# Optimization experiments

Measured on AMD Instinct MI355X. Metric: run time of the kernel, lower is better.

## Reference

```python
import jax, jax.numpy as jnp
import numpy as np

N_NODES = 100000
N_EDGES = 640000
IN_DIM = 64
HID = 128
NUM_GRAPHS = 128
MPNN_STEPS = 3
S2S_STEPS = 3


def setup_inputs() -> dict:
    key = jax.random.key(0)
    ks = jax.random.split(key, 20)
    x = jax.random.normal(ks[0], (N_NODES, IN_DIM), dtype=jnp.float32)
    edge_index = jax.random.randint(ks[1], (2, N_EDGES), 0, N_NODES, dtype=jnp.int32)
    batch = jnp.sort(jax.random.randint(ks[2], (N_NODES,), 0, NUM_GRAPHS, dtype=jnp.int32))
    s = 1.0 / np.sqrt(HID)
    params = {
        # input layer Linear(64 -> 128)
        'W_in': jax.random.normal(ks[3], (HID, IN_DIM), dtype=jnp.float32) * s,
        'b_in': jax.random.normal(ks[4], (HID,), dtype=jnp.float32) * s,
        # MGU parameters (torch.randn init in source)
        'W_f': jax.random.normal(ks[5], (HID, HID), dtype=jnp.float32),
        'U_f': jax.random.normal(ks[6], (HID, HID), dtype=jnp.float32),
        'b_f': jax.random.normal(ks[7], (HID,), dtype=jnp.float32),
        'W_h': jax.random.normal(ks[8], (HID, HID), dtype=jnp.float32),
        'U_h': jax.random.normal(ks[9], (HID, HID), dtype=jnp.float32),
        'b_h': jax.random.normal(ks[10], (HID,), dtype=jnp.float32),
        # Set2Set LSTM: input 2*HID, hidden HID, gate order i,f,g,o
        'lstm_w_ih': jax.random.normal(ks[11], (4 * HID, 2 * HID), dtype=jnp.float32) * s,
        'lstm_w_hh': jax.random.normal(ks[12], (4 * HID, HID), dtype=jnp.float32) * s,
        'lstm_b_ih': jax.random.normal(ks[13], (4 * HID,), dtype=jnp.float32) * s,
        'lstm_b_hh': jax.random.normal(ks[14], (4 * HID,), dtype=jnp.float32) * s,
        # prediction layer Linear(2*HID -> 1)
        'W_pred': jax.random.normal(ks[15], (1, 2 * HID), dtype=jnp.float32) * s,
        'b_pred': jax.random.normal(ks[16], (1,), dtype=jnp.float32) * s,
    }
    return {'x': x, 'edge_index': edge_index, 'batch': batch, **params}


def _mpnn_mgu(h, src, dst, W_f, U_f, b_f, W_h, U_h, b_h):
    # sum-aggregate neighbor messages: m_i = sum_{j->i} h_j
    m = jax.ops.segment_sum(h[src], dst, num_segments=N_NODES)  # [N, H]
    f_t = jax.nn.sigmoid(m @ W_f.T + h @ U_f.T + b_f)
    h_hat = jnp.tanh(m @ W_h.T + (f_t * h) @ U_h.T + b_h)
    return (1.0 - f_t) * h + f_t * h_hat


def _set2set(x, batch, w_ih, w_hh, b_ih, b_hh):
    G, H = NUM_GRAPHS, HID
    q_star = jnp.zeros((G, 2 * H), dtype=x.dtype)
    h_l = jnp.zeros((G, H), dtype=x.dtype)
    c_l = jnp.zeros((G, H), dtype=x.dtype)
    for _ in range(S2S_STEPS):
        gates = q_star @ w_ih.T + h_l @ w_hh.T + b_ih + b_hh  # [G, 4H]
        i, f, g, o = jnp.split(gates, 4, axis=-1)
        c_l = jax.nn.sigmoid(f) * c_l + jax.nn.sigmoid(i) * jnp.tanh(g)
        h_l = jax.nn.sigmoid(o) * jnp.tanh(c_l)
        q = h_l  # [G, H]
        # attention over nodes within each graph segment
        e = jnp.sum(x * q[batch], axis=-1)  # [N]
        e_max = jax.ops.segment_max(e, batch, num_segments=G)
        a_un = jnp.exp(e - e_max[batch])
        denom = jax.ops.segment_sum(a_un, batch, num_segments=G)
        a = a_un / denom[batch]
        r = jax.ops.segment_sum(a[:, None] * x, batch, num_segments=G)  # [G, H]
        q_star = jnp.concatenate([q, r], axis=-1)
    return q_star


def reference(x, edge_index, batch, W_in, b_in, W_f, U_f, b_f, W_h, U_h, b_h,
              lstm_w_ih, lstm_w_hh, lstm_b_ih, lstm_b_hh, W_pred, b_pred):
    h = jax.nn.relu(x @ W_in.T + b_in)  # [N, HID]
    src, dst = edge_index[0], edge_index[1]
    for _ in range(MPNN_STEPS):
        h = _mpnn_mgu(h, src, dst, W_f, U_f, b_f, W_h, U_h, b_h)
    q_star = _set2set(h, batch, lstm_w_ih, lstm_w_hh, lstm_b_ih, lstm_b_hh)  # [G, 2H]
    return q_star @ W_pred.T + b_pred  # [G, 1]
```

## Files before the change

kernel.cpp:

```cpp
#include <hip/hip_runtime.h>
#include <math.h>

#define N_NODES 100000
#define N_EDGES 640000
#define IN_DIM 64
#define HID 128
#define NGRAPH 128

typedef __bf16 bf16x2 __attribute__((ext_vector_type(2)));
typedef __bf16 bf16x4 __attribute__((ext_vector_type(4)));
typedef __bf16 bf16x8 __attribute__((ext_vector_type(8)));
typedef float f32x4 __attribute__((ext_vector_type(4)));

#define LDST 136

__device__ __forceinline__ float sigmoid_f(float z) {
  return __fdividef(1.f, 1.f + __expf(-z));
}
__device__ __forceinline__ float tanh_f(float z) {
  return 1.f - __fdividef(2.f, __expf(2.f * z) + 1.f);
}

__device__ __forceinline__ void fma44(const float4 A[4], const float4 B[4], float acc[4][4]) {
#pragma unroll
  for (int i2 = 0; i2 < 4; ++i2) {
    acc[i2][0] += A[i2].x*B[0].x + A[i2].y*B[1].x + A[i2].z*B[2].x + A[i2].w*B[3].x;
    acc[i2][1] += A[i2].x*B[0].y + A[i2].y*B[1].y + A[i2].z*B[2].y + A[i2].w*B[3].y;
    acc[i2][2] += A[i2].x*B[0].z + A[i2].y*B[1].z + A[i2].z*B[2].z + A[i2].w*B[3].z;
    acc[i2][3] += A[i2].x*B[0].w + A[i2].y*B[1].w + A[i2].z*B[2].w + A[i2].w*B[3].w;
  }
}

__global__ __launch_bounds__(256) void k_input(const float* __restrict__ x,
                                               const float* __restrict__ W,
                                               const float* __restrict__ b,
                                               float* __restrict__ h) {
  __shared__ float wS[64][132];
  __shared__ float xS[32][68];
  int t = threadIdx.x;
  int nb = blockIdx.x * 32;
#pragma unroll
  for (int i = 0; i < 8; ++i) {
    int idx4 = i * 256 + t;
    int j = idx4 >> 4, kq = idx4 & 15;
    float4 v = ((const float4*)W)[j * 16 + kq];
    wS[4*kq+0][j] = v.x; wS[4*kq+1][j] = v.y; wS[4*kq+2][j] = v.z; wS[4*kq+3][j] = v.w;
  }
#pragma unroll
  for (int i = 0; i < 2; ++i) {
    int idx4 = i * 256 + t;
    int n = idx4 >> 4, kq = idx4 & 15;
    float4 v = ((const float4*)x)[(nb + n) * 16 + kq];
    *((float4*)&xS[n][4*kq]) = v;
  }
  __syncthreads();
  int bq = t & 31, a = t >> 5;
  float acc[4][4] = {};
#pragma unroll
  for (int kk4 = 0; kk4 < 16; ++kk4) {
    float4 A[4], B[4];
#pragma unroll
    for (int i2 = 0; i2 < 4; ++i2) A[i2] = *((const float4*)&xS[4*a+i2][4*kk4]);
#pragma unroll
    for (int c = 0; c < 4; ++c) B[c] = *((const float4*)&wS[4*kk4+c][4*bq]);
    fma44(A, B, acc);
  }
  float4 bb = ((const float4*)b)[bq];
  float ba[4] = {bb.x, bb.y, bb.z, bb.w};
#pragma unroll
  for (int i2 = 0; i2 < 4; ++i2) {
    float4 o;
    o.x = fmaxf(acc[i2][0] + ba[0], 0.f);
    o.y = fmaxf(acc[i2][1] + ba[1], 0.f);
    o.z = fmaxf(acc[i2][2] + ba[2], 0.f);
    o.w = fmaxf(acc[i2][3] + ba[3], 0.f);
    ((float4*)h)[(nb + 4*a + i2) * 32 + bq] = o;
  }
}

__global__ __launch_bounds__(256) void k_hist(const int* __restrict__ dst,
                                              int* __restrict__ deg) {
  int e = blockIdx.x * 256 + threadIdx.x;
  if (e < N_EDGES) atomicAdd(&deg[dst[e]], 1);
}

#define SCAN_CHUNK 4096
#define SCAN_NB 25

__global__ __launch_bounds__(256) void k_scan_part(const int* __restrict__ deg,
                                                   int* __restrict__ bsum) {
  __shared__ int red[256];
  int t = threadIdx.x, b = blockIdx.x;
  int base = b * SCAN_CHUNK + t * 16;
  int s = 0;
#pragma unroll
  for (int i = 0; i < 16; ++i) {
    int idx = base + i;
    if (idx < N_NODES) s += deg[idx];
  }
  red[t] = s;
  __syncthreads();
  for (int off = 128; off > 0; off >>= 1) {
    if (t < off) red[t] += red[t + off];
    __syncthreads();
  }
  if (t == 0) bsum[b] = red[0];
}

__global__ void k_scan_mid(const int* __restrict__ bsum, int* __restrict__ boff,
                           int* __restrict__ rowstart) {
  if (threadIdx.x == 0) {
    int run = 0;
    for (int i = 0; i < SCAN_NB; ++i) { boff[i] = run; run += bsum[i]; }
    rowstart[N_NODES] = run;
  }
}

__global__ __launch_bounds__(256) void k_scan_final(const int* __restrict__ deg,
                                                    const int* __restrict__ boff,
                                                    int* __restrict__ rowstart) {
  __shared__ int ts[256];
  int t = threadIdx.x, b = blockIdx.x;
  int base = b * SCAN_CHUNK + t * 16;
  int v[16];
  int s = 0;
#pragma unroll
  for (int i = 0; i < 16; ++i) {
    int idx = base + i;
    v[i] = (idx < N_NODES) ? deg[idx] : 0;
    s += v[i];
  }
  ts[t] = s;
  __syncthreads();
  for (int off = 1; off < 256; off <<= 1) {
    int add = (t >= off) ? ts[t - off] : 0;
    __syncthreads();
    ts[t] += add;
    __syncthreads();
  }
  int run = boff[b] + ts[t] - s;
#pragma unroll
  for (int i = 0; i < 16; ++i) {
    int idx = base + i;
    if (idx < N_NODES) rowstart[idx] = run;
    run += v[i];
  }
}

__global__ __launch_bounds__(256) void k_fill(const int* __restrict__ src,
                                              const int* __restrict__ dst,
                                              int* __restrict__ cursor,
                                              int* __restrict__ srcSorted) {
  int e = blockIdx.x * 256 + threadIdx.x;
  if (e >= N_EDGES) return;
  int d = dst[e];
  int p = atomicAdd(&cursor[d], 1);
  srcSorted[p] = src[e];
}

__global__ __launch_bounds__(256) void k_wsplit(const float* __restrict__ W0,
                                                const float* __restrict__ W1,
                                                const float* __restrict__ W2,
                                                const float* __restrict__ W3,
                                                __bf16* __restrict__ Whi,
                                                __bf16* __restrict__ Wlo) {
  int id = blockIdx.x * 256 + threadIdx.x;
  int mat = id >> 14, idx = id & 16383;
  const float* W = (mat == 0) ? W0 : (mat == 1) ? W1 : (mat == 2) ? W2 : W3;
  float v = W[idx];
  __bf16 hi = (__bf16)v;
  Whi[id] = hi;
  Wlo[id] = (__bf16)(v - (float)hi);
}

__global__ __launch_bounds__(256) void k_gather(const float* __restrict__ h,
                                                const int* __restrict__ rowstart,
                                                const int* __restrict__ srcSorted,
                                                float* __restrict__ m) {
  int node = blockIdx.x * 8 + (threadIdx.x >> 5);
  if (node >= N_NODES) return;
  int li = threadIdx.x & 31;
  int j0 = rowstart[node], j1 = rowstart[node + 1];
  const float4* h4 = (const float4*)h;
  float4 a0 = {0.f, 0.f, 0.f, 0.f}, a1 = {0.f, 0.f, 0.f, 0.f};
  int j = j0;
  for (; j + 1 < j1; j += 2) {
    int s0 = srcSorted[j], s1 = srcSorted[j + 1];
    float4 v0 = h4[s0 * 32 + li];
    float4 v1 = h4[s1 * 32 + li];
    a0.x += v0.x; a0.y += v0.y; a0.z += v0.z; a0.w += v0.w;
    a1.x += v1.x; a1.y += v1.y; a1.z += v1.z; a1.w += v1.w;
  }
  if (j < j1) {
    int s0 = srcSorted[j];
    float4 v0 = h4[s0 * 32 + li];
    a0.x += v0.x; a0.y += v0.y; a0.z += v0.z; a0.w += v0.w;
  }
  float4 o = {a0.x + a1.x, a0.y + a1.y, a0.z + a1.z, a0.w + a1.w};
  ((float4*)m)[node * 32 + li] = o;
}

__global__ __launch_bounds__(256) void k_mgu(float* __restrict__ h,
                                             const float* __restrict__ m,
                                             const __bf16* __restrict__ Whi,
                                             const __bf16* __restrict__ Wlo,
                                             const float* __restrict__ bfp,
                                             const float* __restrict__ bhp) {
  __shared__ __bf16 mHi[64 * LDST], mLo[64 * LDST];
  __shared__ __bf16 hHi[64 * LDST], hLo[64 * LDST];
  const int t = threadIdx.x;
  const int nb = blockIdx.x * 64;

#pragma unroll
  for (int i = 0; i < 8; ++i) {
    int idx4 = i * 256 + t;
    int n = idx4 >> 5, kq = idx4 & 31;
    float4 vm = ((const float4*)m)[(nb + n) * 32 + kq];
    float4 vh = ((const float4*)h)[(nb + n) * 32 + kq];
    bf16x4 mh, ml, hh, hl;
    mh[0] = (__bf16)vm.x; ml[0] = (__bf16)(vm.x - (float)mh[0]);
    mh[1] = (__bf16)vm.y; ml[1] = (__bf16)(vm.y - (float)mh[1]);
    mh[2] = (__bf16)vm.z; ml[2] = (__bf16)(vm.z - (float)mh[2]);
    mh[3] = (__bf16)vm.w; ml[3] = (__bf16)(vm.w - (float)mh[3]);
    hh[0] = (__bf16)vh.x; hl[0] = (__bf16)(vh.x - (float)hh[0]);
    hh[1] = (__bf16)vh.y; hl[1] = (__bf16)(vh.y - (float)hh[1]);
    hh[2] = (__bf16)vh.z; hl[2] = (__bf16)(vh.z - (float)hh[2]);
    hh[3] = (__bf16)vh.w; hl[3] = (__bf16)(vh.w - (float)hh[3]);
    int e0 = n * LDST + 4 * kq;
    *(bf16x4*)&mHi[e0] = mh; *(bf16x4*)&mLo[e0] = ml;
    *(bf16x4*)&hHi[e0] = hh; *(bf16x4*)&hLo[e0] = hl;
  }
  __syncthreads();

  const int w = t >> 6, l = t & 63;
  const int lj = l & 15, q = l >> 4;

  float bfj[2], bhj[2];
#pragma unroll
  for (int ct = 0; ct < 2; ++ct) {
    int j = (2 * w + ct) * 16 + lj;
    bfj[ct] = bfp[j];
    bhj[ct] = bhp[j];
  }

  f32x4 acc[4][2] = {};

#pragma unroll
  for (int kc = 0; kc < 128; kc += 32) {
    bf16x8 bwh[2], bwl[2], buh[2], bul[2];
#pragma unroll
    for (int ct = 0; ct < 2; ++ct) {
      int off = ((2 * w + ct) * 16 + lj) * 128 + kc + q * 8;
      bwh[ct] = *(const bf16x8*)&Whi[off];
      bwl[ct] = *(const bf16x8*)&Wlo[off];
      buh[ct] = *(const bf16x8*)&Whi[16384 + off];
      bul[ct] = *(const bf16x8*)&Wlo[16384 + off];
    }
#pragma unroll
    for (int rt = 0; rt < 4; ++rt) {
      int e0 = (rt * 16 + lj) * LDST + kc + q * 8;
      bf16x8 amh = *(const bf16x8*)&mHi[e0];
      bf16x8 aml = *(const bf16x8*)&mLo[e0];
      bf16x8 ahh = *(const bf16x8*)&hHi[e0];
      bf16x8 ahl = *(const bf16x8*)&hLo[e0];
#pragma unroll
      for (int ct = 0; ct < 2; ++ct) {
        f32x4 a = acc[rt][ct];
        a = __builtin_amdgcn_mfma_f32_16x16x32_bf16(amh, bwh[ct], a, 0, 0, 0);
        a = __builtin_amdgcn_mfma_f32_16x16x32_bf16(amh, bwl[ct], a, 0, 0, 0);
        a = __builtin_amdgcn_mfma_f32_16x16x32_bf16(aml, bwh[ct], a, 0, 0, 0);
        a = __builtin_amdgcn_mfma_f32_16x16x32_bf16(ahh, buh[ct], a, 0, 0, 0);
        a = __builtin_amdgcn_mfma_f32_16x16x32_bf16(ahh, bul[ct], a, 0, 0, 0);
        a = __builtin_amdgcn_mfma_f32_16x16x32_bf16(ahl, buh[ct], a, 0, 0, 0);
        acc[rt][ct] = a;
      }
    }
  }

  __syncthreads();
  float fv[4][2][4], hvv[4][2][4];
#pragma unroll
  for (int rt = 0; rt < 4; ++rt)
#pragma unroll
    for (int ct = 0; ct < 2; ++ct) {
      int j = (2 * w + ct) * 16 + lj;
#pragma unroll
      for (int r = 0; r < 4; ++r) {
        int nl = rt * 16 + q * 4 + r;
        float z = acc[rt][ct][r] + bfj[ct];
        float f = sigmoid_f(z);
        int he = nl * LDST + j;
        float hval = (float)hHi[he] + (float)hLo[he];
        float g = f * hval;
        __bf16 ghi = (__bf16)g;
        hHi[he] = ghi;
        hLo[he] = (__bf16)(g - (float)ghi);
        fv[rt][ct][r] = f;
        hvv[rt][ct][r] = hval;
        acc[rt][ct][r] = 0.f;
      }
    }
  __syncthreads();

#pragma unroll
  for (int kc = 0; kc < 128; kc += 32) {
    bf16x8 bwh[2], bwl[2], buh[2], bul[2];
#pragma unroll
    for (int ct = 0; ct < 2; ++ct) {
      int off = ((2 * w + ct) * 16 + lj) * 128 + kc + q * 8;
      bwh[ct] = *(const bf16x8*)&Whi[2 * 16384 + off];
      bwl[ct] = *(const bf16x8*)&Wlo[2 * 16384 + off];
      buh[ct] = *(const bf16x8*)&Whi[3 * 16384 + off];
      bul[ct] = *(const bf16x8*)&Wlo[3 * 16384 + off];
    }
#pragma unroll
    for (int rt = 0; rt < 4; ++rt) {
      int e0 = (rt * 16 + lj) * LDST + kc + q * 8;
      bf16x8 amh = *(const bf16x8*)&mHi[e0];
      bf16x8 aml = *(const bf16x8*)&mLo[e0];
      bf16x8 agh = *(const bf16x8*)&hHi[e0];
      bf16x8 agl = *(const bf16x8*)&hLo[e0];
#pragma unroll
      for (int ct = 0; ct < 2; ++ct) {
        f32x4 a = acc[rt][ct];
        a = __builtin_amdgcn_mfma_f32_16x16x32_bf16(amh, bwh[ct], a, 0, 0, 0);
        a = __builtin_amdgcn_mfma_f32_16x16x32_bf16(amh, bwl[ct], a, 0, 0, 0);
        a = __builtin_amdgcn_mfma_f32_16x16x32_bf16(aml, bwh[ct], a, 0, 0, 0);
        a = __builtin_amdgcn_mfma_f32_16x16x32_bf16(agh, buh[ct], a, 0, 0, 0);
        a = __builtin_amdgcn_mfma_f32_16x16x32_bf16(agh, bul[ct], a, 0, 0, 0);
        a = __builtin_amdgcn_mfma_f32_16x16x32_bf16(agl, buh[ct], a, 0, 0, 0);
        acc[rt][ct] = a;
      }
    }
  }

#pragma unroll
  for (int rt = 0; rt < 4; ++rt)
#pragma unroll
    for (int ct = 0; ct < 2; ++ct) {
      int j = (2 * w + ct) * 16 + lj;
#pragma unroll
      for (int r = 0; r < 4; ++r) {
        float T = tanh_f(acc[rt][ct][r] + bhj[ct]);
        float f = fv[rt][ct][r];
        float hn = (1.f - f) * hvv[rt][ct][r] + f * T;
        h[(nb + rt * 16 + q * 4 + r) * 128 + j] = hn;
      }
    }
}

__global__ __launch_bounds__(1024) void k_s2s(const float* __restrict__ h,
                                              const int* __restrict__ batch,
                                              const float* __restrict__ w_ih,
                                              const float* __restrict__ w_hh,
                                              const float* __restrict__ b_ih,
                                              const float* __restrict__ b_hh,
                                              const float* __restrict__ Wp,
                                              const float* __restrict__ bp,
                                              float* __restrict__ out) {
  const int g = blockIdx.x, t = threadIdx.x;
  const int w = t >> 6, l = t & 63;
  const int half = l >> 5, li = l & 31;
  const int hw = 2 * w + half;
  __shared__ float qs[256];
  __shared__ float hl[128], cl[128];
  __shared__ float gates[512];
  __shared__ float redM[32], redS[32], scl[32];
  __shared__ float rPart[32][132];
  __shared__ float gInvS;
  __shared__ int bnd[2];

  if (t < 2) {
    int tgt = g + t;
    int lo = 0, hi = N_NODES;
    while (lo < hi) { int mid = (lo + hi) >> 1; if (batch[mid] < tgt) lo = mid + 1; else hi = mid; }
    bnd[t] = lo;
  }
  if (t < 256) qs[t] = 0.f;
  if (t < 128) { hl[t] = 0.f; cl[t] = 0.f; }
  __syncthreads();
  const int s0 = bnd[0], s1 = bnd[1];

  for (int step = 0; step < 3; ++step) {
#pragma unroll 2
    for (int jt = w; jt < 512; jt += 16) {
      const float* wi = w_ih + jt * 256;
      const float* wh = w_hh + jt * 128;
      float s = qs[l] * wi[l] + qs[l+64] * wi[l+64]
              + qs[l+128] * wi[l+128] + qs[l+192] * wi[l+192]
              + hl[l] * wh[l] + hl[l+64] * wh[l+64];
#pragma unroll
      for (int o = 32; o > 0; o >>= 1) s += __shfl_xor(s, o, 64);
      if (l == 0) gates[jt] = s + b_ih[jt] + b_hh[jt];
    }
    __syncthreads();
    if (t < 128) {
      float gi = gates[t], gf = gates[128 + t], gg = gates[256 + t], go = gates[384 + t];
      float c = sigmoid_f(gf) * cl[t] + sigmoid_f(gi) * tanh_f(gg);
      float hh = sigmoid_f(go) * tanh_f(c);
      cl[t] = c;
      hl[t] = hh;
      qs[t] = hh;
    }
    __syncthreads();

    float mw = -INFINITY, sw = 0.f;
    float4 racc = {0.f, 0.f, 0.f, 0.f};
    const float4* h4 = (const float4*)h;
    const float q0 = qs[4*li], q1 = qs[4*li+1], q2 = qs[4*li+2], q3 = qs[4*li+3];
    int n = s0 + hw;
    for (; n + 32 < s1; n += 64) {
      float4 hv0 = h4[n * 32 + li];
      float4 hv1 = h4[(n + 32) * 32 + li];
      float v0 = hv0.x * q0 + hv0.y * q1 + hv0.z * q2 + hv0.w * q3;
      float v1 = hv1.x * q0 + hv1.y * q1 + hv1.z * q2 + hv1.w * q3;
#pragma unroll
      for (int o = 16; o > 0; o >>= 1) {
        v0 += __shfl_xor(v0, o, 64);
        v1 += __shfl_xor(v1, o, 64);
      }
      float nm = fmaxf(mw, fmaxf(v0, v1));
      float sc = __expf(mw - nm);
      float w0 = __expf(v0 - nm);
      float w1 = __expf(v1 - nm);
      sw = sw * sc + w0 + w1;
      racc.x = racc.x * sc + w0 * hv0.x + w1 * hv1.x;
      racc.y = racc.y * sc + w0 * hv0.y + w1 * hv1.y;
      racc.z = racc.z * sc + w0 * hv0.z + w1 * hv1.z;
      racc.w = racc.w * sc + w0 * hv0.w + w1 * hv1.w;
      mw = nm;
    }
    for (; n < s1; n += 32) {
      float4 hv = h4[n * 32 + li];
      float v = hv.x * q0 + hv.y * q1 + hv.z * q2 + hv.w * q3;
#pragma unroll
      for (int o = 16; o > 0; o >>= 1) v += __shfl_xor(v, o, 64);
      float nm = fmaxf(mw, v);
      float sc = __expf(mw - nm);
      float wg = __expf(v - nm);
      sw = sw * sc + wg;
      racc.x = racc.x * sc + wg * hv.x;
      racc.y = racc.y * sc + wg * hv.y;
      racc.z = racc.z * sc + wg * hv.z;
      racc.w = racc.w * sc + wg * hv.w;
      mw = nm;
    }
    if (li == 0) { redM[hw] = mw; redS[hw] = sw; }
    *(float4*)&rPart[hw][4 * li] = racc;
    __syncthreads();
    if (t == 0) {
      float M = -INFINITY;
      for (int i = 0; i < 32; ++i) M = fmaxf(M, redM[i]);
      float S = 0.f;
      for (int i = 0; i < 32; ++i) {
        float s_ = (redM[i] > -INFINITY && M > -INFINITY) ? __expf(redM[i] - M) : 0.f;
        scl[i] = s_;
        S += redS[i] * s_;
      }
      gInvS = (S > 0.f) ? __fdividef(1.f, S) : 0.f;
    }
    __syncthreads();
    if (t < 128) {
      float inv = gInvS;
      float r = 0.f;
#pragma unroll
      for (int i = 0; i < 32; ++i) r += rPart[i][t] * scl[i];
      qs[128 + t] = r * inv;
    }
    __syncthreads();
  }

  __shared__ float pr[256];
  if (t < 256) pr[t] = qs[t] * Wp[t];
  __syncthreads();
  if (t < 128) pr[t] += pr[t + 128];
  __syncthreads();
  if (t < 64) {
    float s = pr[t] + pr[t + 64];
#pragma unroll
    for (int o = 32; o > 0; o >>= 1) s += __shfl_xor(s, o, 64);
    if (t == 0) out[g] = s + bp[0];
  }
}

extern "C" void kernel_launch(void* const* d_in, const int* in_sizes, int n_in,
                              void* d_out, int out_size, void* d_ws, size_t ws_size,
                              hipStream_t stream) {
  const float* x      = (const float*)d_in[0];
  const int*   ei     = (const int*)d_in[1];
  const int*   batch  = (const int*)d_in[2];
  const float* W_in   = (const float*)d_in[3];
  const float* b_in   = (const float*)d_in[4];
  const float* W_f    = (const float*)d_in[5];
  const float* U_f    = (const float*)d_in[6];
  const float* b_f    = (const float*)d_in[7];
  const float* W_h    = (const float*)d_in[8];
  const float* U_h    = (const float*)d_in[9];
  const float* b_h    = (const float*)d_in[10];
  const float* w_ih   = (const float*)d_in[11];
  const float* w_hh   = (const float*)d_in[12];
  const float* b_ih   = (const float*)d_in[13];
  const float* b_hh   = (const float*)d_in[14];
  const float* W_pred = (const float*)d_in[15];
  const float* b_pred = (const float*)d_in[16];
  float* out = (float*)d_out;

  char* ws = (char*)d_ws;
  float* h      = (float*)(ws);
  float* m      = (float*)(ws + 51200000);
  int*   rowstart = (int*)(ws + 103063808);
  int*   srcSorted= (int*)(ws + 103463824);
  int*   bsum   = (int*)  (ws + 106023824);
  int*   boff   = (int*)  (ws + 106023936);
  int*    deg    = (int*)(ws + 102400000);
  int*    cursor = (int*)(ws + 102400000);
  __bf16* Whi    = (__bf16*)(ws + 102400000);
  __bf16* Wlo    = (__bf16*)(ws + 102531072);

  const int* src = ei;
  const int* dst = ei + N_EDGES;

  hipMemsetAsync(deg, 0, N_NODES * 4, stream);
  k_hist<<<(N_EDGES + 255) / 256, 256, 0, stream>>>(dst, deg);
  k_scan_part<<<SCAN_NB, 256, 0, stream>>>(deg, bsum);
  k_scan_mid<<<1, 32, 0, stream>>>(bsum, boff, rowstart);
  k_scan_final<<<SCAN_NB, 256, 0, stream>>>(deg, boff, rowstart);
  hipMemcpyAsync(cursor, rowstart, N_NODES * 4, hipMemcpyDeviceToDevice, stream);
  k_fill<<<(N_EDGES + 255) / 256, 256, 0, stream>>>(src, dst, cursor, srcSorted);

  k_wsplit<<<256, 256, 0, stream>>>(W_f, U_f, W_h, U_h, Whi, Wlo);

  k_input<<<N_NODES / 32, 256, 0, stream>>>(x, W_in, b_in, h);

  for (int step = 0; step < 3; ++step) {
    k_gather<<<(N_NODES + 7) / 8, 256, 0, stream>>>(h, rowstart, srcSorted, m);
    k_mgu<<<(N_NODES + 63) / 64, 256, 0, stream>>>(h, m, Whi, Wlo, b_f, b_h);
  }

  k_s2s<<<NGRAPH, 1024, 0, stream>>>(h, batch, w_ih, w_hh, b_ih, b_hh,
                                     W_pred, b_pred, out);
}
```

Before: 721.8 us.

## Batch Set2Set LSTM gates across graphs with split-bf16 MFMA GEMM

Splits the monolithic per-graph Set2Set kernel into separate per-step kernels: a batched gate GEMM, an LSTM cell kernel, an attention kernel, and a final prediction kernel. The LSTM gate computation runs as one batched [128 x 384] by [384 x 512] GEMM on MFMA, using a three-term hi/lo bf16 split to keep near-fp32 accuracy. Previously every graph block re-read the full LSTM weights from global memory for a scalar matvec. The cost is about ten extra kernel launches, plus round trips of state through global memory between steps.

```diff
diff --git a/kernel.cpp b/kernel.cpp
--- a/kernel.cpp
+++ b/kernel.cpp
@@ -13,6 +13,8 @@
 typedef float f32x4 __attribute__((ext_vector_type(4)));
 
 #define LDST 136
+#define KCAT 384
+#define KPAD 392
 
 __device__ __forceinline__ float sigmoid_f(float z) {
   return __fdividef(1.f, 1.f + __expf(-z));
@@ -171,6 +173,18 @@
   __bf16 hi = (__bf16)v;
   Whi[id] = hi;
   Wlo[id] = (__bf16)(v - (float)hi);
+}
+
+__global__ void k_wsplit2(const float* __restrict__ w_ih,
+                          const float* __restrict__ w_hh,
+                          __bf16* __restrict__ WcHi,
+                          __bf16* __restrict__ WcLo) {
+  int j = blockIdx.x;
+  int k = threadIdx.x;
+  float v = (k < 256) ? w_ih[j * 256 + k] : w_hh[j * 128 + (k - 256)];
+  __bf16 hi = (__bf16)v;
+  WcHi[j * KCAT + k] = hi;
+  WcLo[j * KCAT + k] = (__bf16)(v - (float)hi);
 }
 
 __global__ __launch_bounds__(256) void k_gather(const float* __restrict__ h,
@@ -349,22 +363,91 @@
     }
 }
 
-__global__ __launch_bounds__(1024) void k_s2s(const float* __restrict__ h,
-                                              const int* __restrict__ batch,
-                                              const float* __restrict__ w_ih,
-                                              const float* __restrict__ w_hh,
+__global__ __launch_bounds__(256) void k_gates(const float* __restrict__ q_star,
+                                               const float* __restrict__ h_l,
+                                               const __bf16* __restrict__ WcHi,
+                                               const __bf16* __restrict__ WcLo,
+                                               float* __restrict__ gates) {
+  __shared__ __bf16 sHi[64 * KPAD], sLo[64 * KPAD];
+  const int t = threadIdx.x, b = blockIdx.x;
+  const int w = t >> 6, l = t & 63, lj = l & 15, q = l >> 4;
+  const int ct = b * 2 + (w & 1);
+  const int rh = w >> 1;
+  const float4* qs4 = (const float4*)q_star;
+  const float4* hl4 = (const float4*)h_l;
+  const int sg = t >> 2, part = t & 3;
+
+  for (int chunk = 0; chunk < 2; ++chunk) {
+    __syncthreads();
+    int g0 = chunk * 64;
+#pragma unroll
+    for (int i = 0; i < 24; ++i) {
+      int k4 = part * 24 + i;
+      float4 v = (k4 < 64) ? qs4[(g0 + sg) * 64 + k4]
+                           : hl4[(g0 + sg) * 32 + (k4 - 64)];
+      bf16x4 hi, lo;
+      hi[0] = (__bf16)v.x; lo[0] = (__bf16)(v.x - (float)hi[0]);
+      hi[1] = (__bf16)v.y; lo[1] = (__bf16)(v.y - (float)hi[1]);
+      hi[2] = (__bf16)v.z; lo[2] = (__bf16)(v.z - (float)hi[2]);
+      hi[3] = (__bf16)v.w; lo[3] = (__bf16)(v.w - (float)hi[3]);
+      int e0 = sg * KPAD + k4 * 4;
+      *(bf16x4*)&sHi[e0] = hi; *(bf16x4*)&sLo[e0] = lo;
+    }
+    __syncthreads();
+    f32x4 acc[2] = {};
+#pragma unroll
+    for (int kc = 0; kc < KCAT; kc += 32) {
+      bf16x8 bh = *(const bf16x8*)&WcHi[(ct * 16 + lj) * KCAT + kc + q * 8];
+      bf16x8 bl = *(const bf16x8*)&WcLo[(ct * 16 + lj) * KCAT + kc + q * 8];
+#pragma unroll
+      for (int rt = 0; rt < 2; ++rt) {
+        int e0 = ((rh * 2 + rt) * 16 + lj) * KPAD + kc + q * 8;
+        bf16x8 ah = *(const bf16x8*)&sHi[e0];
+        bf16x8 al = *(const bf16x8*)&sLo[e0];
+        f32x4 a = acc[rt];
+        a = __builtin_amdgcn_mfma_f32_16x16x32_bf16(ah, bh, a, 0, 0, 0);
+        a = __builtin_amdgcn_mfma_f32_16x16x32_bf16(ah, bl, a, 0, 0, 0);
+        a = __builtin_amdgcn_mfma_f32_16x16x32_bf16(al, bh, a, 0, 0, 0);
+        acc[rt] = a;
+      }
+    }
+    int j = ct * 16 + lj;
+#pragma unroll
+    for (int rt = 0; rt < 2; ++rt)
+#pragma unroll
+      for (int r = 0; r < 4; ++r) {
+        int g = g0 + (rh * 2 + rt) * 16 + q * 4 + r;
+        gates[g * 512 + j] = acc[rt][r];
+      }
+  }
+}
+
+__global__ __launch_bounds__(256) void k_cell(const float* __restrict__ gates,
                                               const float* __restrict__ b_ih,
                                               const float* __restrict__ b_hh,
-                                              const float* __restrict__ Wp,
-                                              const float* __restrict__ bp,
-                                              float* __restrict__ out) {
+                                              float* __restrict__ q_star,
+                                              float* __restrict__ h_l,
+                                              float* __restrict__ c_l) {
+  int id = blockIdx.x * 256 + threadIdx.x;
+  int g = id >> 7, hu = id & 127;
+  float gi = gates[g * 512 + hu]       + b_ih[hu]       + b_hh[hu];
+  float gf = gates[g * 512 + 128 + hu] + b_ih[128 + hu] + b_hh[128 + hu];
+  float gg = gates[g * 512 + 256 + hu] + b_ih[256 + hu] + b_hh[256 + hu];
+  float go = gates[g * 512 + 384 + hu] + b_ih[384 + hu] + b_hh[384 + hu];
+  float c = sigmoid_f(gf) * c_l[id] + sigmoid_f(gi) * tanh_f(gg);
+  float hh = sigmoid_f(go) * tanh_f(c);
+  c_l[id] = c;
+  h_l[id] = hh;
+  q_star[g * 256 + hu] = hh;
+}
+
+__global__ __launch_bounds__(1024) void k_attn(const float* __restrict__ h,
+                                               const int* __restrict__ batch,
+                                               float* __restrict__ q_star) {
   const int g = blockIdx.x, t = threadIdx.x;
   const int w = t >> 6, l = t & 63;
   const int half = l >> 5, li = l & 31;
   const int hw = 2 * w + half;
-  __shared__ float qs[256];
-  __shared__ float hl[128], cl[128];
-  __shared__ float gates[512];
   __shared__ float redM[32], redS[32], scl[32];
   __shared__ float rPart[32][132];
   __shared__ float gInvS;
@@ -376,111 +459,82 @@
     while (lo < hi) { int mid = (lo + hi) >> 1; if (batch[mid] < tgt) lo = mid + 1; else hi = mid; }
     bnd[t] = lo;
   }
-  if (t < 256) qs[t] = 0.f;
-  if (t < 128) { hl[t] = 0.f; cl[t] = 0.f; }
   __syncthreads();
   const int s0 = bnd[0], s1 = bnd[1];
 
-  for (int step = 0; step < 3; ++step) {
-#pragma unroll 2
-    for (int jt = w; jt < 512; jt += 16) {
-      const float* wi = w_ih + jt * 256;
-      const float* wh = w_hh + jt * 128;
-      float s = qs[l] * wi[l] + qs[l+64] * wi[l+64]
-              + qs[l+128] * wi[l+128] + qs[l+192] * wi[l+192]
-              + hl[l] * wh[l] + hl[l+64] * wh[l+64];
-#pragma unroll
-      for (int o = 32; o > 0; o >>= 1) s += __shfl_xor(s, o, 64);
-      if (l == 0) gates[jt] = s + b_ih[jt] + b_hh[jt];
-    }
-    __syncthreads();
-    if (t < 128) {
-      float gi = gates[t], gf = gates[128 + t], gg = gates[256 + t], go = gates[384 + t];
-      float c = sigmoid_f(gf) * cl[t] + sigmoid_f(gi) * tanh_f(gg);
-      float hh = sigmoid_f(go) * tanh_f(c);
-      cl[t] = c;
-      hl[t] = hh;
-      qs[t] = hh;
-    }
-    __syncthreads();
-
-    float mw = -INFINITY, sw = 0.f;
-    float4 racc = {0.f, 0.f, 0.f, 0.f};
-    const float4* h4 = (const float4*)h;
-    const float q0 = qs[4*li], q1 = qs[4*li+1], q2 = qs[4*li+2], q3 = qs[4*li+3];
-    int n = s0 + hw;
-    for (; n + 32 < s1; n += 64) {
-      float4 hv0 = h4[n * 32 + li];
-      float4 hv1 = h4[(n + 32) * 32 + li];
-      float v0 = hv0.x * q0 + hv0.y * q1 + hv0.z * q2 + hv0.w * q3;
-      float v1 = hv1.x * q0 + hv1.y * q1 + hv1.z * q2 + hv1.w * q3;
-#pragma unroll
-      for (int o = 16; o > 0; o >>= 1) {
-        v0 += __shfl_xor(v0, o, 64);
-        v1 += __shfl_xor(v1, o, 64);
-      }
-      float nm = fmaxf(mw, fmaxf(v0, v1));
-      float sc = __expf(mw - nm);
-      float w0 = __expf(v0 - nm);
-      float w1 = __expf(v1 - nm);
-      sw = sw * sc + w0 + w1;
-      racc.x = racc.x * sc + w0 * hv0.x + w1 * hv1.x;
-      racc.y = racc.y * sc + w0 * hv0.y + w1 * hv1.y;
-      racc.z = racc.z * sc + w0 * hv0.z + w1 * hv1.z;
-      racc.w = racc.w * sc + w0 * hv0.w + w1 * hv1.w;
-      mw = nm;
-    }
-    for (; n < s1; n += 32) {
-      float4 hv = h4[n * 32 + li];
-      float v = hv.x * q0 + hv.y * q1 + hv.z * q2 + hv.w * q3;
-#pragma unroll
-      for (int o = 16; o > 0; o >>= 1) v += __shfl_xor(v, o, 64);
-      float nm = fmaxf(mw, v);
-      float sc = __expf(mw - nm);
-      float wg = __expf(v - nm);
-      sw = sw * sc + wg;
-      racc.x = racc.x * sc + wg * hv.x;
-      racc.y = racc.y * sc + wg * hv.y;
-      racc.z = racc.z * sc + wg * hv.z;
-      racc.w = racc.w * sc + wg * hv.w;
-      mw = nm;
-    }
-    if (li == 0) { redM[hw] = mw; redS[hw] = sw; }
-    *(float4*)&rPart[hw][4 * li] = racc;
-    __syncthreads();
-    if (t == 0) {
-      float M = -INFINITY;
-      for (int i = 0; i < 32; ++i) M = fmaxf(M, redM[i]);
-      float S = 0.f;
-      for (int i = 0; i < 32; ++i) {
-        float s_ = (redM[i] > -INFINITY && M > -INFINITY) ? __expf(redM[i] - M) : 0.f;
-        scl[i] = s_;
-        S += redS[i] * s_;
-      }
-      gInvS = (S > 0.f) ? __fdividef(1.f, S) : 0.f;
-    }
-    __syncthreads();
-    if (t < 128) {
-      float inv = gInvS;
-      float r = 0.f;
-#pragma unroll
-      for (int i = 0; i < 32; ++i) r += rPart[i][t] * scl[i];
-      qs[128 + t] = r * inv;
-    }
-    __syncthreads();
-  }
-
-  __shared__ float pr[256];
-  if (t < 256) pr[t] = qs[t] * Wp[t];
-  __syncthreads();
-  if (t < 128) pr[t] += pr[t + 128];
-  __syncthreads();
-  if (t < 64) {
-    float s = pr[t] + pr[t + 64];
-#pragma unroll
-    for (int o = 32; o > 0; o >>= 1) s += __shfl_xor(s, o, 64);
-    if (t == 0) out[g] = s + bp[0];
-  }
+  float4 qv = ((const float4*)q_star)[g * 64 + li];
+  const float q0 = qv.x, q1 = qv.y, q2 = qv.z, q3 = qv.w;
+
+  float mw = -INFINITY, sw = 0.f;
+  float4 racc = {0.f, 0.f, 0.f, 0.f};
+  const float4* h4 = (const float4*)h;
+  int n = s0 + hw;
+  for (; n + 32 < s1; n += 64) {
+    float4 hv0 = h4[n * 32 + li];
+    float4 hv1 = h4[(n + 32) * 32 + li];
+    float v0 = hv0.x * q0 + hv0.y * q1 + hv0.z * q2 + hv0.w * q3;
+    float v1 = hv1.x * q0 + hv1.y * q1 + hv1.z * q2 + hv1.w * q3;
+#pragma unroll
+    for (int o = 16; o > 0; o >>= 1) {
+      v0 += __shfl_xor(v0, o, 64);
+      v1 += __shfl_xor(v1, o, 64);
+    }
+    float nm = fmaxf(mw, fmaxf(v0, v1));
+    float sc = __expf(mw - nm);
+    float w0 = __expf(v0 - nm);
+    float w1 = __expf(v1 - nm);
+    sw = sw * sc + w0 + w1;
+    racc.x = racc.x * sc + w0 * hv0.x + w1 * hv1.x;
+    racc.y = racc.y * sc + w0 * hv0.y + w1 * hv1.y;
+    racc.z = racc.z * sc + w0 * hv0.z + w1 * hv1.z;
+    racc.w = racc.w * sc + w0 * hv0.w + w1 * hv1.w;
+    mw = nm;
+  }
+  for (; n < s1; n += 32) {
+    float4 hv = h4[n * 32 + li];
+    float v = hv.x * q0 + hv.y * q1 + hv.z * q2 + hv.w * q3;
+#pragma unroll
+    for (int o = 16; o > 0; o >>= 1) v += __shfl_xor(v, o, 64);
+    float nm = fmaxf(mw, v);
+    float sc = __expf(mw - nm);
+    float wg = __expf(v - nm);
+    sw = sw * sc + wg;
+    racc.x = racc.x * sc + wg * hv.x;
+    racc.y = racc.y * sc + wg * hv.y;
+    racc.z = racc.z * sc + wg * hv.z;
+    racc.w = racc.w * sc + wg * hv.w;
+    mw = nm;
+  }
+  if (li == 0) { redM[hw] = mw; redS[hw] = sw; }
+  *(float4*)&rPart[hw][4 * li] = racc;
+  __syncthreads();
+  if (t == 0) {
+    float M = -INFINITY;
+    for (int i = 0; i < 32; ++i) M = fmaxf(M, redM[i]);
+    float S = 0.f;
+    for (int i = 0; i < 32; ++i) {
+      float s_ = (redM[i] > -INFINITY && M > -INFINITY) ? __expf(redM[i] - M) : 0.f;
+      scl[i] = s_;
+      S += redS[i] * s_;
+    }
+    gInvS = (S > 0.f) ? __fdividef(1.f, S) : 0.f;
+  }
+  __syncthreads();
+  if (t < 128) {
+    float inv = gInvS;
+    float r = 0.f;
+#pragma unroll
+    for (int i = 0; i < 32; ++i) r += rPart[i][t] * scl[i];
+    q_star[g * 256 + 128 + t] = r * inv;
+  }
+}
+
+__global__ void k_pred(const float* __restrict__ q_star, const float* __restrict__ Wp,
+                       const float* __restrict__ bp, float* __restrict__ out) {
+  int g = threadIdx.x;
+  float s = 0.f;
+  for (int k = 0; k < 256; ++k) s += q_star[g * 256 + k] * Wp[k];
+  out[g] = s + bp[0];
 }
 
 extern "C" void kernel_launch(void* const* d_in, const int* in_sizes, int n_in,
@@ -516,6 +570,13 @@
   int*    cursor = (int*)(ws + 102400000);
   __bf16* Whi    = (__bf16*)(ws + 102400000);
   __bf16* Wlo    = (__bf16*)(ws + 102531072);
+  char* mB = (char*)m;
+  __bf16* WcHi   = (__bf16*)(mB);
+  __bf16* WcLo   = (__bf16*)(mB + 393216);
+  float*  gates  = (float*)(mB + 786432);
+  float*  q_star = (float*)(mB + 1048576);
+  float*  h_l    = (float*)(mB + 1179648);
+  float*  c_l    = (float*)(mB + 1245184);
 
   const int* src = ei;
   const int* dst = ei + N_EDGES;
@@ -537,6 +598,14 @@
     k_mgu<<<(N_NODES + 63) / 64, 256, 0, stream>>>(h, m, Whi, Wlo, b_f, b_h);
   }
 
-  k_s2s<<<NGRAPH, 1024, 0, stream>>>(h, batch, w_ih, w_hh, b_ih, b_hh,
-                                     W_pred, b_pred, out);
-}
+  k_wsplit2<<<512, KCAT, 0, stream>>>(w_ih, w_hh, WcHi, WcLo);
+  hipMemsetAsync(q_star, 0, 262144, stream);
+
+  for (int s = 0; s < 3; ++s) {
+    k_gates<<<16, 256, 0, stream>>>(q_star, h_l, WcHi, WcLo, gates);
+    k_cell<<<64, 256, 0, stream>>>(gates, b_ih, b_hh, q_star, h_l, c_l);
+    k_attn<<<NGRAPH, 1024, 0, stream>>>(h, batch, q_star);
+  }
+
+  k_pred<<<1, 128, 0, stream>>>(q_star, W_pred, b_pred, out);
+}
```

Result: no change. 729.6 us (+1.1%).
